# Optimization experiments

Measured on AMD Instinct MI355X. Metric: run time of the kernel, lower is better.

The kernel has to match this reference:

```python
import jax, jax.numpy as jnp
import numpy as np

N = 50000      # num nodes
E = 400000     # num edges
D = 384        # input_dim
H = 4          # heads
C = 128        # hidden_dim per head
HC = H * C     # 512


def setup_inputs() -> dict:
    key = jax.random.key(0)
    ks = jax.random.split(key, 32)
    w = lambda k, shape: jax.random.normal(k, shape, jnp.float32) * 0.05
    inp = {
        "x": jax.random.normal(ks[0], (N, D), jnp.float32),
        "edge_index": jax.random.randint(ks[1], (2, E), 0, N, dtype=jnp.int32),
    }
    dims = [(D, HC), (HC, HC)]  # layer0 in=384, layer1 in=512
    i = 2
    for l, (din, dout) in enumerate(dims):
        for nm in ["q", "k", "v", "s"]:  # query/key/value/skip linears
            inp[f"{nm}{l}_w"] = w(ks[i], (dout, din)); i += 1
            inp[f"{nm}{l}_b"] = jnp.zeros((dout,), jnp.float32)
    inp["out_w"] = w(ks[i], (D, HC))
    inp["out_b"] = jnp.zeros((D,), jnp.float32)
    return inp


def _transformer_conv(x, src, dst, Wq, bq, Wk, bk, Wv, bv, Ws, bs):
    # PyG TransformerConv, concat=True, root_weight=True, no edge features.
    n = x.shape[0]
    q = (x @ Wq.T + bq).reshape(n, H, C)
    k = (x @ Wk.T + bk).reshape(n, H, C)
    v = (x @ Wv.T + bv).reshape(n, H, C)
    # per-edge attention logits [E, H]; target = dst, source = src
    alpha = (q[dst] * k[src]).sum(-1) / jnp.sqrt(jnp.float32(C))
    m = jax.ops.segment_max(alpha, dst, num_segments=n)
    m = jnp.where(jnp.isfinite(m), m, 0.0)  # nodes with no in-edges
    e = jnp.exp(alpha - m[dst])
    denom = jax.ops.segment_sum(e, dst, num_segments=n)
    a = e / (denom[dst] + 1e-16)             # segment softmax [E, H]
    msg = v[src] * a[:, :, None]             # [E, H, C]
    agg = jax.ops.segment_sum(msg, dst, num_segments=n).reshape(n, HC)
    return agg + x @ Ws.T + bs               # + root/skip connection


def reference(x, edge_index,
              q0_w, q0_b, k0_w, k0_b, v0_w, v0_b, s0_w, s0_b,
              q1_w, q1_b, k1_w, k1_b, v1_w, v1_b, s1_w, s1_b,
              out_w, out_b):
    src, dst = edge_index[0], edge_index[1]
    h = _transformer_conv(x, src, dst, q0_w, q0_b, k0_w, k0_b, v0_w, v0_b, s0_w, s0_b)
    h = jax.nn.relu(h)
    h = _transformer_conv(h, src, dst, q1_w, q1_b, k1_w, k1_b, v1_w, v1_b, s1_w, s1_b)
    h = jax.nn.relu(h)
    return h @ out_w.T + out_b  # [N, D]
```

## Files before the change

kernel.cpp:

```cpp
#include <hip/hip_runtime.h>
#include <hip/hip_bf16.h>

#define NN 50000
#define NE 400000
#define DD 384
#define HC 512

typedef unsigned int u32;
typedef unsigned short u16;
typedef __attribute__((ext_vector_type(8))) short bf16x8;
typedef __attribute__((ext_vector_type(4))) float f32x4;

#define AS1 __attribute__((address_space(1)))
#define AS3 __attribute__((address_space(3)))

__device__ __forceinline__ float bflo(u32 u){ return __uint_as_float(u << 16); }
__device__ __forceinline__ float bfhi(u32 u){ return __uint_as_float(u & 0xFFFF0000u); }
__device__ __forceinline__ u16 f2bf(float f){
    u32 u = __float_as_uint(f);
    return (u16)((u + 0x7FFFu + ((u >> 16) & 1u)) >> 16);
}
__device__ __forceinline__ u32 pack2(float a, float b){
    return (u32)f2bf(a) | ((u32)f2bf(b) << 16);
}

template<int K>
__global__ __launch_bounds__(512)
void gemm_ws(const u16* __restrict__ Ab, const u16* __restrict__ Wb,
             const float* __restrict__ bias,
             u16* __restrict__ oQ, u16* __restrict__ oK,
             u16* __restrict__ oV, u16* __restrict__ oS)
{
    constexpr int NKC  = K / 32;
    constexpr int WCH  = K / 8;
    constexpr int NPAN = (NN + 255) / 256;
    __shared__ char smW[128 * K * 2];
    __shared__ char smA[2][16384];

    const int b   = blockIdx.x;
    const int xcd = b & 7;
    const int idx = b >> 3;
    const int ct  = idx & 15;
    const int rh  = idx >> 4;

    const int tid  = threadIdx.x;
    const int lane = tid & 63;
    const int w    = tid >> 6;
    const int wr   = w >> 1;
    const int wc   = w & 1;
    const int r16  = lane & 15;
    const int kq   = lane >> 4;

    {
        const u16* W0 = Wb + (size_t)ct * 128 * K;
        #pragma unroll
        for (int p = 0; p < (128 * WCH) / 512; ++p) {
            int ci = p * 512 + tid;
            int row = ci / WCH, pc = ci % WCH;
            int lc = (pc & ~7) | ((pc ^ row) & 7);
            __builtin_amdgcn_global_load_lds((const AS1 u32*)(W0 + (size_t)row * K + lc * 8),
                                             (AS3 u32*)(smW + (size_t)ci * 16), 16, 0, 0);
        }
    }

    int np = 0;
    while ((2 * np + rh) * 8 + xcd < NPAN) ++np;
    const int total = np * NKC;

    auto stageA = [&](int t) {
        int jp = t / NKC, kc = t - jp * NKC;
        int m0 = ((2 * jp + rh) * 8 + xcd) * 256;
        #pragma unroll
        for (int p = 0; p < 2; ++p) {
            int ci = p * 512 + tid;
            int row = ci >> 2, pc = ci & 3;
            int lc = (pc - (row >> 1)) & 3;
            int gr = m0 + row; if (gr >= NN) gr = NN - 1;
            __builtin_amdgcn_global_load_lds((const AS1 u32*)(Ab + (size_t)gr * K + kc * 32 + lc * 8),
                                             (AS3 u32*)(smA[t & 1] + ci * 16), 16, 0, 0);
        }
    };

    stageA(0);
    if (total > 1) stageA(1);

    f32x4 acc[4][4] = {};

    const int qsel = ct >> 2;
    u16* outp = (qsel == 0) ? oQ : (qsel == 1) ? oK : (qsel == 2) ? oV : oS;
    const int cb = (ct & 3) * 128 + wc * 64;
    float bv4[4];
    #pragma unroll
    for (int ni = 0; ni < 4; ++ni) bv4[ni] = bias[ct * 128 + wc * 64 + ni * 16 + r16];

    for (int t = 0; t < total; ++t) {
        const int jp = t / NKC, kc = t - jp * NKC;
        if (t + 1 >= total)          { asm volatile("s_waitcnt vmcnt(0)"  ::: "memory"); }
        else if (kc <= 1 && t > 1)   { asm volatile("s_waitcnt vmcnt(63)" ::: "memory"); }
        else                         { asm volatile("s_waitcnt vmcnt(2)"  ::: "memory"); }
        __builtin_amdgcn_s_barrier();
        __builtin_amdgcn_sched_barrier(0);

        const char* bufA = smA[t & 1];
        const int c = kc * 4 + kq;
        const int wbase = (c & ~7) << 4;
        bf16x8 av[4], bv[4];
        #pragma unroll
        for (int i = 0; i < 4; ++i) {
            int rowA = wr * 64 + i * 16 + r16;
            av[i] = *(const bf16x8*)(bufA + rowA * 64 + (((kq + (rowA >> 1)) & 3) << 4));
        }
        #pragma unroll
        for (int i = 0; i < 4; ++i) {
            int rowW = wc * 64 + i * 16 + r16;
            bv[i] = *(const bf16x8*)(smW + (size_t)rowW * (K * 2) + wbase
                                     + (((c ^ rowW) & 7) << 4));
        }
        #pragma unroll
        for (int mi = 0; mi < 4; ++mi)
            #pragma unroll
            for (int ni = 0; ni < 4; ++ni)
                acc[mi][ni] = __builtin_amdgcn_mfma_f32_16x16x32_bf16(
                    av[mi], bv[ni], acc[mi][ni], 0, 0, 0);

        __builtin_amdgcn_sched_barrier(0);
        __builtin_amdgcn_s_barrier();
        __builtin_amdgcn_sched_barrier(0);

        if (t + 2 < total) stageA(t + 2);

        if (kc == NKC - 1) {
            int m0 = ((2 * jp + rh) * 8 + xcd) * 256;
            #pragma unroll
            for (int mi = 0; mi < 4; ++mi) {
                #pragma unroll
                for (int ni = 0; ni < 4; ++ni) {
                    int col = cb + ni * 16 + r16;
                    float bb = bv4[ni];
                    #pragma unroll
                    for (int r = 0; r < 4; ++r) {
                        int gr = m0 + wr * 64 + mi * 16 + kq * 4 + r;
                        if (gr < NN) outp[(size_t)gr * 512 + col] = f2bf(acc[mi][ni][r] + bb);
                        acc[mi][ni][r] = 0.f;
                    }
                }
            }
        }
    }
}

template<int K>
__global__ __launch_bounds__(256)
void gemm2ph(const u16* __restrict__ Ab, const u16* __restrict__ Wb,
             const float* __restrict__ bias, float* __restrict__ oF,
             int n, int Ototal, int NT)
{
    constexpr int NKT = K / 64;
    __shared__ char smA[2][16384];
    __shared__ char smB[2][16384];

    const int nb  = gridDim.x;
    const int bd  = blockIdx.x;
    const int q8  = nb >> 3, r8 = nb & 7;
    const int xcd = bd & 7, gg = bd >> 3;
    const int tt  = (xcd < r8 ? xcd * (q8 + 1) : r8 * (q8 + 1) + (xcd - r8) * q8) + gg;
    const int m0  = (tt / NT) * 128;
    const int o0  = (tt % NT) * 128;

    const int tid  = threadIdx.x;
    const int lane = tid & 63;
    const int w    = tid >> 6;
    const int wr   = w >> 1, wc = w & 1;
    const int r16  = lane & 15;
    const int kq   = lane >> 4;
    const int swz  = (r16 & 7) << 4;

    auto stage = [&](int bf, int kt) {
        #pragma unroll
        for (int p = 0; p < 4; ++p) {
            int ci = p * 256 + tid, row = ci >> 3, pc = ci & 7;
            int lc = pc ^ (row & 7);
            const u16* g = Wb + (size_t)(o0 + row) * K + kt * 64 + lc * 8;
            __builtin_amdgcn_global_load_lds((const AS1 u32*)g,
                                             (AS3 u32*)(smB[bf] + ci * 16), 16, 0, 0);
        }
        #pragma unroll
        for (int p = 0; p < 4; ++p) {
            int ci = p * 256 + tid, row = ci >> 3, pc = ci & 7;
            int lc = pc ^ (row & 7);
            int gr = m0 + row; if (gr >= n) gr = n - 1;
            const u16* g = Ab + (size_t)gr * K + kt * 64 + lc * 8;
            __builtin_amdgcn_global_load_lds((const AS1 u32*)g,
                                             (AS3 u32*)(smA[bf] + ci * 16), 16, 0, 0);
        }
    };

    f32x4 acc[4][4] = {};

    stage(0, 0);
    stage(1, 1);

    for (int kt = 0; kt < NKT; ++kt) {
        if (kt + 1 < NKT) { asm volatile("s_waitcnt vmcnt(8)" ::: "memory"); }
        else             { asm volatile("s_waitcnt vmcnt(0)" ::: "memory"); }
        __builtin_amdgcn_s_barrier();
        __builtin_amdgcn_sched_barrier(0);

        const char* pa = smA[kt & 1] + (wr * 64) * 128;
        const char* pb = smB[kt & 1] + (wc * 64) * 128;
        #pragma unroll
        for (int kk = 0; kk < 2; ++kk) {
            const int kb = kk * 64 + kq * 16;
            bf16x8 av[4], bv[4];
            #pragma unroll
            for (int i = 0; i < 4; ++i) {
                av[i] = *(const bf16x8*)(pa + (i * 16 + r16) * 128 + (kb ^ swz));
                bv[i] = *(const bf16x8*)(pb + (i * 16 + r16) * 128 + (kb ^ swz));
            }
            #pragma unroll
            for (int mi = 0; mi < 4; ++mi)
                #pragma unroll
                for (int ni = 0; ni < 4; ++ni)
                    acc[mi][ni] = __builtin_amdgcn_mfma_f32_16x16x32_bf16(
                        av[mi], bv[ni], acc[mi][ni], 0, 0, 0);
        }

        __builtin_amdgcn_sched_barrier(0);
        __builtin_amdgcn_s_barrier();
        __builtin_amdgcn_sched_barrier(0);
        if (kt + 2 < NKT) stage(kt & 1, kt + 2);
    }

    const int cbo = o0 + wc * 64;
    #pragma unroll
    for (int ni = 0; ni < 4; ++ni) {
        int col = cbo + ni * 16 + r16;
        float bb = bias[col];
        #pragma unroll
        for (int mi = 0; mi < 4; ++mi)
            #pragma unroll
            for (int r = 0; r < 4; ++r) {
                int gr = m0 + wr * 64 + mi * 16 + kq * 4 + r;
                if (gr < n) oF[(size_t)gr * Ototal + col] = acc[mi][ni][r] + bb;
            }
    }
}

#define XG  2400000
#define W0G 24576
#define W1G 32768
#define WOG 24576
#define CVT_TOTAL (XG + 4*W0G + 4*W1G + WOG)

__global__ __launch_bounds__(256)
void cvt_all(const float* __restrict__ x,
             const float* q0w, const float* k0w, const float* v0w, const float* s0w,
             const float* q1w, const float* k1w, const float* v1w, const float* s1w,
             const float* ow,
             u16* __restrict__ Xb, u16* __restrict__ Wc0,
             u16* __restrict__ Wc1, u16* __restrict__ WcO)
{
    int i = blockIdx.x * 256 + threadIdx.x;
    if (i >= CVT_TOTAL) return;
    const float* s; u16* d; int g;
    if (i < XG) { s = x; d = Xb; g = i; }
    else {
        int j = i - XG;
        if (j < 4 * W0G) {
            int q = j / W0G; g = j - q * W0G;
            s = (q == 0 ? q0w : q == 1 ? k0w : q == 2 ? v0w : s0w);
            d = Wc0 + (size_t)q * W0G * 8;
        } else if ((j -= 4 * W0G) < 4 * W1G) {
            int q = j / W1G; g = j - q * W1G;
            s = (q == 0 ? q1w : q == 1 ? k1w : q == 2 ? v1w : s1w);
            d = Wc1 + (size_t)q * W1G * 8;
        } else { j -= 4 * W1G; s = ow; d = WcO; g = j; }
    }
    float4 f0 = ((const float4*)s)[(size_t)g * 2];
    float4 f1 = ((const float4*)s)[(size_t)g * 2 + 1];
    uint4 o;
    o.x = pack2(f0.x, f0.y); o.y = pack2(f0.z, f0.w);
    o.z = pack2(f1.x, f1.y); o.w = pack2(f1.z, f1.w);
    ((uint4*)d)[g] = o;
}

__global__ __launch_bounds__(256)
void pack_bias(const float* q0, const float* k0, const float* v0, const float* s0,
               const float* q1, const float* k1, const float* v1, const float* s1,
               const float* ob, float* __restrict__ dst)
{
    int i = blockIdx.x * 256 + threadIdx.x;
    if (i >= 4480) return;
    float v;
    if (i < 2048) {
        int j = i & 511, q = i >> 9;
        v = (q == 0 ? q0 : q == 1 ? k0 : q == 2 ? v0 : s0)[j];
    } else if (i < 4096) {
        int j = i - 2048; int q = j >> 9; j &= 511;
        v = (q == 0 ? q1 : q == 1 ? k1 : q == 2 ? v1 : s1)[j];
    } else {
        v = ob[i - 4096];
    }
    dst[i] = v;
}

__global__ __launch_bounds__(256)
void zero_deg(int* __restrict__ deg)
{
    int i = blockIdx.x * 256 + threadIdx.x;
    if (i < NN) deg[i] = 0;
}

__global__ __launch_bounds__(256)
void hist_dst(const int* __restrict__ dst, int* __restrict__ deg)
{
    int e = blockIdx.x * 256 + threadIdx.x;
    if (e < NE) atomicAdd(&deg[dst[e]], 1);
}

__global__ __launch_bounds__(1024)
void scan_deg(const int* __restrict__ deg, int* __restrict__ rowptr,
              int* __restrict__ cursor)
{
    __shared__ int wsum[16];
    const int tid = threadIdx.x, lane = tid & 63, wid = tid >> 6;
    int carry = 0;
    for (int base = 0; base < NN; base += 1024) {
        int i = base + tid;
        int orig = (i < NN) ? deg[i] : 0;
        int v = orig;
        #pragma unroll
        for (int off = 1; off < 64; off <<= 1) {
            int t = __shfl_up(v, off, 64);
            if (lane >= off) v += t;
        }
        if (lane == 63) wsum[wid] = v;
        __syncthreads();
        if (wid == 0) {
            int s = (lane < 16) ? wsum[lane] : 0;
            #pragma unroll
            for (int off = 1; off < 16; off <<= 1) {
                int t = __shfl_up(s, off, 16);
                if ((lane & 15) >= off) s += t;
            }
            if (lane < 16) wsum[lane] = s;
        }
        __syncthreads();
        int woff  = (wid == 0) ? 0 : wsum[wid - 1];
        int total = wsum[15];
        int excl  = carry + woff + (v - orig);
        if (i < NN) { rowptr[i] = excl; cursor[i] = excl; }
        carry += total;
        __syncthreads();
    }
    if (tid == 0) rowptr[NN] = NE;
}

__global__ __launch_bounds__(256)
void scatter_edges(const int* __restrict__ src, const int* __restrict__ dst,
                   int* __restrict__ cursor, int* __restrict__ esrc_ord)
{
    int e = blockIdx.x * 256 + threadIdx.x;
    if (e >= NE) return;
    int pos = atomicAdd(&cursor[dst[e]], 1);
    esrc_ord[pos] = src[e];
}

__global__ __launch_bounds__(256)
void node_attn(const u16* __restrict__ Qb, const u16* __restrict__ Kb,
               const u16* __restrict__ Vb, const int* __restrict__ rowptr,
               const int* __restrict__ esrc, const u16* __restrict__ skipb,
               u16* __restrict__ outb)
{
    int d = blockIdx.x * 4 + (threadIdx.x >> 6);
    if (d >= NN) return;
    int lane = threadIdx.x & 63;

    uint4 qv = *((const uint4*)(Qb + (size_t)d * HC) + lane);
    float q[8] = { bflo(qv.x), bfhi(qv.x), bflo(qv.y), bfhi(qv.y),
                   bflo(qv.z), bfhi(qv.z), bflo(qv.w), bfhi(qv.w) };

    int beg = rowptr[d], end = rowptr[d + 1];
    float m = -INFINITY, den = 0.f;
    float acc[8] = {};

    if (beg < end) {
        int s0 = esrc[beg];
        uint4 kv = *((const uint4*)(Kb + (size_t)s0 * HC) + lane);
        uint4 vv = *((const uint4*)(Vb + (size_t)s0 * HC) + lane);

        for (int i = beg; i < end; ++i) {
            uint4 kc = kv, vc = vv;
            if (i + 1 < end) {
                int sn = esrc[i + 1];
                kv = *((const uint4*)(Kb + (size_t)sn * HC) + lane);
                vv = *((const uint4*)(Vb + (size_t)sn * HC) + lane);
            }
            float sum = q[0] * bflo(kc.x) + q[1] * bfhi(kc.x)
                      + q[2] * bflo(kc.y) + q[3] * bfhi(kc.y)
                      + q[4] * bflo(kc.z) + q[5] * bfhi(kc.z)
                      + q[6] * bflo(kc.w) + q[7] * bfhi(kc.w);
            #pragma unroll
            for (int off = 1; off < 16; off <<= 1) sum += __shfl_xor(sum, off, 64);
            float alpha = sum * 0.08838834764831845f;

            float mnew  = fmaxf(m, alpha);
            float scale = __expf(m - mnew);
            float p     = __expf(alpha - mnew);
            den = den * scale + p;

            acc[0] = acc[0] * scale + p * bflo(vc.x);
            acc[1] = acc[1] * scale + p * bfhi(vc.x);
            acc[2] = acc[2] * scale + p * bflo(vc.y);
            acc[3] = acc[3] * scale + p * bfhi(vc.y);
            acc[4] = acc[4] * scale + p * bflo(vc.z);
            acc[5] = acc[5] * scale + p * bfhi(vc.z);
            acc[6] = acc[6] * scale + p * bflo(vc.w);
            acc[7] = acc[7] * scale + p * bfhi(vc.w);
            m = mnew;
        }
    }

    float inv = 1.f / (den + 1e-16f);
    size_t base = (size_t)d * HC + lane * 8;
    uint4 sv = *((const uint4*)(skipb + base));
    float sk[8] = { bflo(sv.x), bfhi(sv.x), bflo(sv.y), bfhi(sv.y),
                    bflo(sv.z), bfhi(sv.z), bflo(sv.w), bfhi(sv.w) };
    uint4 o;
    o.x = pack2(fmaxf(acc[0] * inv + sk[0], 0.f), fmaxf(acc[1] * inv + sk[1], 0.f));
    o.y = pack2(fmaxf(acc[2] * inv + sk[2], 0.f), fmaxf(acc[3] * inv + sk[3], 0.f));
    o.z = pack2(fmaxf(acc[4] * inv + sk[4], 0.f), fmaxf(acc[5] * inv + sk[5], 0.f));
    o.w = pack2(fmaxf(acc[6] * inv + sk[6], 0.f), fmaxf(acc[7] * inv + sk[7], 0.f));
    *(uint4*)(outb + base) = o;
}

extern "C" void kernel_launch(void* const* d_in, const int* in_sizes, int n_in,
                              void* d_out, int out_size, void* d_ws, size_t ws_size,
                              hipStream_t stream)
{
    const float* x   = (const float*)d_in[0];
    const int* ei    = (const int*)d_in[1];
    const int* esrc  = ei;
    const int* edst  = ei + NE;
    const float* q0w = (const float*)d_in[2];  const float* q0b = (const float*)d_in[3];
    const float* k0w = (const float*)d_in[4];  const float* k0b = (const float*)d_in[5];
    const float* v0w = (const float*)d_in[6];  const float* v0b = (const float*)d_in[7];
    const float* s0w = (const float*)d_in[8];  const float* s0b = (const float*)d_in[9];
    const float* q1w = (const float*)d_in[10]; const float* q1b = (const float*)d_in[11];
    const float* k1w = (const float*)d_in[12]; const float* k1b = (const float*)d_in[13];
    const float* v1w = (const float*)d_in[14]; const float* v1b = (const float*)d_in[15];
    const float* s1w = (const float*)d_in[16]; const float* s1b = (const float*)d_in[17];
    const float* ow  = (const float*)d_in[18]; const float* obs = (const float*)d_in[19];

    char* p = (char*)d_ws;
    auto take = [&](size_t bytes) { void* r = (void*)p; p += (bytes + 255) & ~(size_t)255; return r; };
    u16*   Qb     = (u16*)take((size_t)NN * HC * 2);
    u16*   Vb     = (u16*)take((size_t)NN * HC * 2);
    u16*   Hb     = (u16*)take((size_t)NN * HC * 2);
    u16*   Sb     = (u16*)take((size_t)NN * HC * 2);
    u16*   Xb     = (u16*)take((size_t)NN * DD * 2);
    u16*   Wc0    = (u16*)take((size_t)2048 * DD * 2);
    u16*   Wc1    = (u16*)take((size_t)2048 * HC * 2);
    u16*   WcO    = (u16*)take((size_t)DD * HC * 2);
    float* barena = (float*)take(4480 * 4);

    char* dob = (char*)d_out;
    u16* Kb       = (u16*)dob;
    int* deg      = (int*)(dob + 51200000);
    int* rowptr   = (int*)(dob + 51400192);
    int* cursor   = (int*)(dob + 51600384);
    int* esrc_ord = (int*)(dob + 51800576);

    dim3 blk(256);
    int gN   = (NN + 255) / 256;
    int gE   = (NE + 255) / 256;
    int gnod = (NN + 3) / 4;
    const int NPAN = (NN + 127) / 128;
    int go = NPAN * 3;

    pack_bias<<<(4480 + 255) / 256, blk, 0, stream>>>(q0b, k0b, v0b, s0b,
                                                      q1b, k1b, v1b, s1b, obs, barena);
    cvt_all<<<(CVT_TOTAL + 255) / 256, blk, 0, stream>>>(x,
        q0w, k0w, v0w, s0w, q1w, k1w, v1w, s1w, ow, Xb, Wc0, Wc1, WcO);

    zero_deg      <<<gN, blk, 0, stream>>>(deg);
    hist_dst      <<<gE, blk, 0, stream>>>(edst, deg);
    scan_deg      <<<1, 1024, 0, stream>>>(deg, rowptr, cursor);
    scatter_edges <<<gE, blk, 0, stream>>>(esrc, edst, cursor, esrc_ord);

    gemm_ws<DD><<<256, 512, 0, stream>>>(Xb, Wc0, barena, Qb, Kb, Vb, Sb);
    node_attn<<<gnod, blk, 0, stream>>>(Qb, Kb, Vb, rowptr, esrc_ord, Sb, Hb);

    gemm_ws<HC><<<256, 512, 0, stream>>>(Hb, Wc1, barena + 2048, Qb, Kb, Vb, Sb);
    node_attn<<<gnod, blk, 0, stream>>>(Qb, Kb, Vb, rowptr, esrc_ord, Sb, Hb);

    gemm2ph<HC><<<go, blk, 0, stream>>>(Hb, WcO, barena + 4096,
                                        (float*)d_out, NN, 384, 3);
}
```

Baseline: 777.0 us.

## Shrink QKVS GEMM row tile and process two edges per attention iteration

Result: faster. 717.0 us (median of 2 runs) (-7.7%).

```diff
diff --git a/kernel.cpp b/kernel.cpp
--- a/kernel.cpp
+++ b/kernel.cpp
@@ -22,6 +22,12 @@
 }
 __device__ __forceinline__ u32 pack2(float a, float b){
     return (u32)f2bf(a) | ((u32)f2bf(b) << 16);
+}
+__device__ __forceinline__ float dot8(const float* q, uint4 k){
+    return q[0] * bflo(k.x) + q[1] * bfhi(k.x)
+         + q[2] * bflo(k.y) + q[3] * bfhi(k.y)
+         + q[4] * bflo(k.z) + q[5] * bfhi(k.z)
+         + q[6] * bflo(k.w) + q[7] * bfhi(k.w);
 }
 
 template<int K>
@@ -31,9 +37,9 @@
              u16* __restrict__ oQ, u16* __restrict__ oK,
              u16* __restrict__ oV, u16* __restrict__ oS)
 {
-    constexpr int NKC  = K / 32;
+    constexpr int NKT  = K / 64;
     constexpr int WCH  = K / 8;
-    constexpr int NPAN = (NN + 255) / 256;
+    constexpr int NPAN = (NN + 127) / 128;
     __shared__ char smW[128 * K * 2];
     __shared__ char smA[2][16384];
 
@@ -46,45 +52,44 @@
     const int tid  = threadIdx.x;
     const int lane = tid & 63;
     const int w    = tid >> 6;
-    const int wr   = w >> 1;
+    const int wq   = w >> 1;
     const int wc   = w & 1;
     const int r16  = lane & 15;
     const int kq   = lane >> 4;
 
-    {
-        const u16* W0 = Wb + (size_t)ct * 128 * K;
-        #pragma unroll
-        for (int p = 0; p < (128 * WCH) / 512; ++p) {
-            int ci = p * 512 + tid;
-            int row = ci / WCH, pc = ci % WCH;
-            int lc = (pc & ~7) | ((pc ^ row) & 7);
-            __builtin_amdgcn_global_load_lds((const AS1 u32*)(W0 + (size_t)row * K + lc * 8),
-                                             (AS3 u32*)(smW + (size_t)ci * 16), 16, 0, 0);
-        }
-    }
-
+    const u16* Wrow0 = Wb + (size_t)ct * 128 * K;
+    #pragma unroll
+    for (int p = 0; p < (128 * WCH) / 512; ++p) {
+        int ci = p * 512 + tid;
+        int row = ci / WCH, pc = ci % WCH;
+        int lc = (pc & ~7) | ((pc ^ row) & 7);
+        __builtin_amdgcn_global_load_lds((const AS1 u32*)(Wrow0 + (size_t)row * K + lc * 8),
+                                         (AS3 u32*)(smW + (size_t)ci * 16), 16, 0, 0);
+    }
+
+    auto panel = [&](int j) { return (2 * j + rh) * 8 + xcd; };
     int np = 0;
-    while ((2 * np + rh) * 8 + xcd < NPAN) ++np;
-    const int total = np * NKC;
+    while (panel(np) < NPAN) ++np;
+    const int total = np * NKT;
 
     auto stageA = [&](int t) {
-        int jp = t / NKC, kc = t - jp * NKC;
-        int m0 = ((2 * jp + rh) * 8 + xcd) * 256;
+        int j = t / NKT, kc = t - (t / NKT) * NKT;
+        int m0 = panel(j) * 128;
         #pragma unroll
         for (int p = 0; p < 2; ++p) {
             int ci = p * 512 + tid;
-            int row = ci >> 2, pc = ci & 3;
-            int lc = (pc - (row >> 1)) & 3;
+            int row = ci >> 3, pc = ci & 7;
+            int lc = pc ^ (row & 7);
             int gr = m0 + row; if (gr >= NN) gr = NN - 1;
-            __builtin_amdgcn_global_load_lds((const AS1 u32*)(Ab + (size_t)gr * K + kc * 32 + lc * 8),
+            __builtin_amdgcn_global_load_lds((const AS1 u32*)(Ab + (size_t)gr * K + kc * 64 + lc * 8),
                                              (AS3 u32*)(smA[t & 1] + ci * 16), 16, 0, 0);
         }
     };
 
     stageA(0);
-    if (total > 1) stageA(1);
-
-    f32x4 acc[4][4] = {};
+    stageA(1);
+
+    f32x4 acc[2][4] = {};
 
     const int qsel = ct >> 2;
     u16* outp = (qsel == 0) ? oQ : (qsel == 1) ? oK : (qsel == 2) ? oV : oS;
@@ -94,58 +99,59 @@
     for (int ni = 0; ni < 4; ++ni) bv4[ni] = bias[ct * 128 + wc * 64 + ni * 16 + r16];
 
     for (int t = 0; t < total; ++t) {
-        const int jp = t / NKC, kc = t - jp * NKC;
-        if (t + 1 >= total)          { asm volatile("s_waitcnt vmcnt(0)"  ::: "memory"); }
-        else if (kc <= 1 && t > 1)   { asm volatile("s_waitcnt vmcnt(63)" ::: "memory"); }
-        else                         { asm volatile("s_waitcnt vmcnt(2)"  ::: "memory"); }
+        if (t + 1 < total) { asm volatile("s_waitcnt vmcnt(2)" ::: "memory"); }
+        else               { asm volatile("s_waitcnt vmcnt(0)" ::: "memory"); }
         __builtin_amdgcn_s_barrier();
         __builtin_amdgcn_sched_barrier(0);
 
+        const int jj = t / NKT;
+        const int kt = t - jj * NKT;
         const char* bufA = smA[t & 1];
-        const int c = kc * 4 + kq;
-        const int wbase = (c & ~7) << 4;
-        bf16x8 av[4], bv[4];
-        #pragma unroll
-        for (int i = 0; i < 4; ++i) {
-            int rowA = wr * 64 + i * 16 + r16;
-            av[i] = *(const bf16x8*)(bufA + rowA * 64 + (((kq + (rowA >> 1)) & 3) << 4));
-        }
-        #pragma unroll
-        for (int i = 0; i < 4; ++i) {
-            int rowW = wc * 64 + i * 16 + r16;
-            bv[i] = *(const bf16x8*)(smW + (size_t)rowW * (K * 2) + wbase
-                                     + (((c ^ rowW) & 7) << 4));
-        }
-        #pragma unroll
-        for (int mi = 0; mi < 4; ++mi)
-            #pragma unroll
-            for (int ni = 0; ni < 4; ++ni)
-                acc[mi][ni] = __builtin_amdgcn_mfma_f32_16x16x32_bf16(
-                    av[mi], bv[ni], acc[mi][ni], 0, 0, 0);
+        #pragma unroll
+        for (int kk = 0; kk < 2; ++kk) {
+            bf16x8 av[2], bv[4];
+            #pragma unroll
+            for (int i = 0; i < 2; ++i) {
+                int rowA = wq * 32 + i * 16 + r16;
+                int c = kk * 4 + kq;
+                av[i] = *(const bf16x8*)(bufA + rowA * 128 + ((c ^ (rowA & 7)) << 4));
+            }
+            #pragma unroll
+            for (int i = 0; i < 4; ++i) {
+                int rowW = wc * 64 + i * 16 + r16;
+                int c = kt * 8 + kk * 4 + kq;
+                int pcw = (c & ~7) | ((c ^ rowW) & 7);
+                bv[i] = *(const bf16x8*)(smW + (size_t)rowW * (K * 2) + (pcw << 4));
+            }
+            #pragma unroll
+            for (int mi = 0; mi < 2; ++mi)
+                #pragma unroll
+                for (int ni = 0; ni < 4; ++ni)
+                    acc[mi][ni] = __builtin_amdgcn_mfma_f32_16x16x32_bf16(
+                        av[mi], bv[ni], acc[mi][ni], 0, 0, 0);
+        }
 
         __builtin_amdgcn_sched_barrier(0);
         __builtin_amdgcn_s_barrier();
         __builtin_amdgcn_sched_barrier(0);
 
-        if (t + 2 < total) stageA(t + 2);
-
-        if (kc == NKC - 1) {
-            int m0 = ((2 * jp + rh) * 8 + xcd) * 256;
-            #pragma unroll
-            for (int mi = 0; mi < 4; ++mi) {
+        if (kt == NKT - 1) {
+            int m0 = panel(jj) * 128;
+            #pragma unroll
+            for (int ni = 0; ni < 4; ++ni) {
+                int col = cb + ni * 16 + r16;
+                float bb = bv4[ni];
                 #pragma unroll
-                for (int ni = 0; ni < 4; ++ni) {
-                    int col = cb + ni * 16 + r16;
-                    float bb = bv4[ni];
+                for (int mi = 0; mi < 2; ++mi)
                     #pragma unroll
                     for (int r = 0; r < 4; ++r) {
-                        int gr = m0 + wr * 64 + mi * 16 + kq * 4 + r;
+                        int gr = m0 + wq * 32 + mi * 16 + kq * 4 + r;
                         if (gr < NN) outp[(size_t)gr * 512 + col] = f2bf(acc[mi][ni][r] + bb);
                         acc[mi][ni][r] = 0.f;
                     }
-                }
             }
         }
+        if (t + 2 < total) stageA(t + 2);
     }
 }
 
@@ -381,44 +387,78 @@
                    bflo(qv.z), bfhi(qv.z), bflo(qv.w), bfhi(qv.w) };
 
     int beg = rowptr[d], end = rowptr[d + 1];
+    int cnt = end - beg;
     float m = -INFINITY, den = 0.f;
     float acc[8] = {};
 
-    if (beg < end) {
-        int s0 = esrc[beg];
-        uint4 kv = *((const uint4*)(Kb + (size_t)s0 * HC) + lane);
-        uint4 vv = *((const uint4*)(Vb + (size_t)s0 * HC) + lane);
-
-        for (int i = beg; i < end; ++i) {
-            uint4 kc = kv, vc = vv;
-            if (i + 1 < end) {
-                int sn = esrc[i + 1];
-                kv = *((const uint4*)(Kb + (size_t)sn * HC) + lane);
-                vv = *((const uint4*)(Vb + (size_t)sn * HC) + lane);
-            }
-            float sum = q[0] * bflo(kc.x) + q[1] * bfhi(kc.x)
-                      + q[2] * bflo(kc.y) + q[3] * bfhi(kc.y)
-                      + q[4] * bflo(kc.z) + q[5] * bfhi(kc.z)
-                      + q[6] * bflo(kc.w) + q[7] * bfhi(kc.w);
-            #pragma unroll
-            for (int off = 1; off < 16; off <<= 1) sum += __shfl_xor(sum, off, 64);
-            float alpha = sum * 0.08838834764831845f;
-
-            float mnew  = fmaxf(m, alpha);
-            float scale = __expf(m - mnew);
-            float p     = __expf(alpha - mnew);
-            den = den * scale + p;
-
-            acc[0] = acc[0] * scale + p * bflo(vc.x);
-            acc[1] = acc[1] * scale + p * bfhi(vc.x);
-            acc[2] = acc[2] * scale + p * bflo(vc.y);
-            acc[3] = acc[3] * scale + p * bfhi(vc.y);
-            acc[4] = acc[4] * scale + p * bflo(vc.z);
-            acc[5] = acc[5] * scale + p * bfhi(vc.z);
-            acc[6] = acc[6] * scale + p * bflo(vc.w);
-            acc[7] = acc[7] * scale + p * bfhi(vc.w);
-            m = mnew;
-        }
+    uint4 k0, v0, k1, v1;
+    if (cnt > 0) {
+        int s = esrc[beg];
+        k0 = *((const uint4*)(Kb + (size_t)s * HC) + lane);
+        v0 = *((const uint4*)(Vb + (size_t)s * HC) + lane);
+    }
+    if (cnt > 1) {
+        int s = esrc[beg + 1];
+        k1 = *((const uint4*)(Kb + (size_t)s * HC) + lane);
+        v1 = *((const uint4*)(Vb + (size_t)s * HC) + lane);
+    }
+
+    int i = beg;
+    for (; i + 1 < end; i += 2) {
+        uint4 ka = k0, va = v0, kb = k1, vb = v1;
+        if (i + 2 < end) {
+            int s = esrc[i + 2];
+            k0 = *((const uint4*)(Kb + (size_t)s * HC) + lane);
+            v0 = *((const uint4*)(Vb + (size_t)s * HC) + lane);
+        }
+        if (i + 3 < end) {
+            int s = esrc[i + 3];
+            k1 = *((const uint4*)(Kb + (size_t)s * HC) + lane);
+            v1 = *((const uint4*)(Vb + (size_t)s * HC) + lane);
+        }
+        float s0 = dot8(q, ka);
+        float s1 = dot8(q, kb);
+        #pragma unroll
+        for (int off = 1; off < 16; off <<= 1) {
+            s0 += __shfl_xor(s0, off, 64);
+            s1 += __shfl_xor(s1, off, 64);
+        }
+        float a0 = s0 * 0.08838834764831845f;
+        float a1 = s1 * 0.08838834764831845f;
+
+        float mnew  = fmaxf(m, fmaxf(a0, a1));
+        float scale = __expf(m - mnew);
+        float p0    = __expf(a0 - mnew);
+        float p1    = __expf(a1 - mnew);
+        den = den * scale + p0 + p1;
+
+        acc[0] = acc[0] * scale + p0 * bflo(va.x) + p1 * bflo(vb.x);
+        acc[1] = acc[1] * scale + p0 * bfhi(va.x) + p1 * bfhi(vb.x);
+        acc[2] = acc[2] * scale + p0 * bflo(va.y) + p1 * bflo(vb.y);
+        acc[3] = acc[3] * scale + p0 * bfhi(va.y) + p1 * bfhi(vb.y);
+        acc[4] = acc[4] * scale + p0 * bflo(va.z) + p1 * bflo(vb.z);
+        acc[5] = acc[5] * scale + p0 * bfhi(va.z) + p1 * bfhi(vb.z);
+        acc[6] = acc[6] * scale + p0 * bflo(va.w) + p1 * bflo(vb.w);
+        acc[7] = acc[7] * scale + p0 * bfhi(va.w) + p1 * bfhi(vb.w);
+        m = mnew;
+    }
+    if (i < end) {
+        float s0 = dot8(q, k0);
+        #pragma unroll
+        for (int off = 1; off < 16; off <<= 1) s0 += __shfl_xor(s0, off, 64);
+        float a0 = s0 * 0.08838834764831845f;
+        float mnew  = fmaxf(m, a0);
+        float scale = __expf(m - mnew);
+        float p0    = __expf(a0 - mnew);
+        den = den * scale + p0;
+        acc[0] = acc[0] * scale + p0 * bflo(v0.x);
+        acc[1] = acc[1] * scale + p0 * bfhi(v0.x);
+        acc[2] = acc[2] * scale + p0 * bflo(v0.y);
+        acc[3] = acc[3] * scale + p0 * bfhi(v0.y);
+        acc[4] = acc[4] * scale + p0 * bflo(v0.z);
+        acc[5] = acc[5] * scale + p0 * bfhi(v0.z);
+        acc[6] = acc[6] * scale + p0 * bflo(v0.w);
+        acc[7] = acc[7] * scale + p0 * bfhi(v0.w);
     }
 
     float inv = 1.f / (den + 1e-16f);
```
